# Performance work log

Hardware: AMD Instinct MI355X
Metric: run time of the kernel (lower is better)

Reference implementation:

```python
import jax, jax.numpy as jnp
import numpy as np

EOS = 0
INCLUDE_EOS = True
INS_COST = 1.0
DEL_COST = 1.0
SUB_COST = 1.0


def _seq_lens(tok):
    # tok: (T, N) int tokens; length = index of first EOS (+1 if included), else T
    T = tok.shape[0]
    is_eos = tok == EOS
    has = is_eos.any(axis=0)
    idx = jnp.argmax(is_eos, axis=0)
    return jnp.where(has, idx + (1 if INCLUDE_EOS else 0), T)


def _edit_distance(ref, hyp, ref_lens, hyp_lens):
    # ref: (R, N), hyp: (H, N). Levenshtein DP, scan over hyp steps.
    # The sequential deletion dependence along the ref axis is turned into a
    # min-plus prefix scan: new_row[j] = j*del + cummin_k<=j (cand[k] - k*del).
    R, N = ref.shape
    H = hyp.shape[0]
    offs = (jnp.arange(R + 1, dtype=jnp.float32) * DEL_COST)[:, None]  # (R+1,1)
    row0 = jnp.broadcast_to(offs, (R + 1, N)) + jnp.zeros((R + 1, N), jnp.float32)

    def step(row, xs):
        i, h = xs  # i: 1-based hyp step, h: (N,) hyp tokens at this step
        sub_c = SUB_COST * (ref != h[None, :]).astype(jnp.float32)  # (R,N)
        cand = jnp.concatenate(
            [row[:1] + INS_COST,
             jnp.minimum(row[1:] + INS_COST, row[:-1] + sub_c)], axis=0)
        new_row = jax.lax.cummin(cand - offs, axis=0) + offs
        # freeze rows for sequences whose hypothesis already ended
        row = jnp.where(i <= hyp_lens[None, :], new_row, row)
        return row, None

    row, _ = jax.lax.scan(step, row0, (jnp.arange(1, H + 1), hyp))
    # distance at (hyp_len, ref_len) per sequence
    return jnp.take_along_axis(row, ref_lens[None, :], axis=0)[0]


def setup_inputs() -> dict:
    key = jax.random.key(0)
    k1, k2, k3 = jax.random.split(key, 3)
    log_probs = jax.random.normal(k1, (128, 64), dtype=jnp.float32)
    ref = jax.random.randint(k2, (256, 128), 0, 1000, dtype=jnp.int64)
    hyp = jax.random.randint(k3, (256, 128, 64), 0, 1000, dtype=jnp.int64)
    return {"log_probs": log_probs, "ref": ref, "hyp": hyp}


def reference(log_probs, ref, hyp):
    batch_size, samples = log_probs.shape
    R = ref.shape[0]
    H = hyp.shape[0]
    # ref is 2D: broadcast across samples (same reference per batch element)
    ref_flat = jnp.repeat(ref[:, :, None], samples, axis=2).reshape(R, batch_size * samples)
    hyp_flat = hyp.reshape(H, batch_size * samples)
    ref_lens = _seq_lens(ref_flat)
    hyp_lens = _seq_lens(hyp_flat)
    dist = _edit_distance(ref_flat, hyp_flat, ref_lens, hyp_lens)
    er = dist / ref_lens.astype(jnp.float32)  # norm=True -> error rate
    er = er.reshape(batch_size, samples)
    er = er - er.mean(axis=1, keepdims=True)  # sub_avg=True
    loss = er * jax.nn.softmax(log_probs, axis=1)
    return loss.mean()  # reduction='mean'
```

## Files before the change

kernel.cpp:

```cpp
#include <hip/hip_runtime.h>
#include <stdint.h>


#define BATCH   128
#define SAMPLES 64
#define RLEN    256
#define HLEN    256
#define NSEQ    (BATCH*SAMPLES)
#define NTOK    1000
#define PADTOK  1000
#define SPB     32
#define PMSTR   9
#define HEADPAD 28
#define TAILPAD 40
#define HTROW   324
#define RSTEP   4
#define NPH     72

typedef unsigned long long u64;
typedef unsigned int       u32;

__device__ __forceinline__ int row_shr1(int x) {
    return __builtin_amdgcn_mov_dpp(x, 0x111, 0xf, 0xf, true);
}

__global__ __launch_bounds__(256) void mer_edit(const int* __restrict__ ref,
                                                const int* __restrict__ hyp,
                                                int* __restrict__ scores,
                                                int* __restrict__ reflen)
{
    const int blk  = blockIdx.x;
    const int b    = blk >> 1;
    const int half = blk & 1;
    const int tid  = threadIdx.x;
    const int w    = tid & 7;
    const int sl   = tid >> 3;

    __shared__ __align__(16) u32 pm[9012];
    __shared__ __align__(8)  unsigned short ht[SPB * HTROW];
    __shared__ int m_sh;

    if (tid == 0) m_sh = RLEN;

    for (int i = tid; i < 2253; i += 256)
        ((int4*)pm)[i] = int4{0, 0, 0, 0};

    {
        const int r = tid >> 3, c = tid & 7;
        u32* rowp = (u32*)ht + r * (HTROW / 2);
#pragma unroll
        for (int j0 = 0; j0 < 5; ++j0) {
            int j = c * 5 + j0;
            if (j < 34) {
                int off = (j < 14) ? j : (142 + (j - 14));
                rowp[off] = 0x03E803E8u;
            }
        }
    }

#pragma unroll
    for (int it = 0; it < 8; it++) {
        int idx = it * 256 + tid;
        int t   = idx >> 3;
        int s4  = (idx & 7) * 4;
        int4 v  = *(const int4*)(hyp + t * NSEQ + b * SAMPLES + half * SPB + s4);
        ht[(s4 + 0) * HTROW + HEADPAD + t] = (unsigned short)v.x;
        ht[(s4 + 1) * HTROW + HEADPAD + t] = (unsigned short)v.y;
        ht[(s4 + 2) * HTROW + HEADPAD + t] = (unsigned short)v.z;
        ht[(s4 + 3) * HTROW + HEADPAD + t] = (unsigned short)v.w;
    }

    const int rt = ref[tid * BATCH + b];
    __syncthreads();
    if (rt == 0) atomicMin(&m_sh, tid);
    __syncthreads();
    const int m = (m_sh < RLEN) ? (m_sh + 1) : RLEN;
    if (tid < m)
        atomicOr(&pm[rt * PMSTR + (tid >> 5)], 1u << (tid & 31));
    __syncthreads();

    const int  sw   = (m - 1) >> 5, sb = (m - 1) & 31;
    const bool isW0 = (w == 0);
    const bool isSW = (w == sw);
    const u32* pmw  = pm + w;
    const unsigned short* htrow = ht + sl * HTROW + HEADPAD;

    u32  VP = ~0u, VN = 0u;
    int  score = m;
    bool done  = false;
    int  base  = -(w << 2);

    uint2 tkA = *(const uint2*)(htrow + base);
    uint2 tkB = *(const uint2*)(htrow + base + 4);
    u32 eqA0, eqA1, eqA2, eqA3;
    {
        u32 p0 = tkA.x & 0xFFFFu, p1 = tkA.x >> 16;
        u32 p2 = tkA.y & 0xFFFFu, p3 = tkA.y >> 16;
        eqA0 = pmw[p0 * PMSTR]; eqA1 = pmw[p1 * PMSTR];
        eqA2 = pmw[p2 * PMSTR]; eqA3 = pmw[p3 * PMSTR];
    }

    int out_pkd = 0;

#define STEP(EQ, TK, I) do {                                              \
        u32 cin  = ((u32)inp >> (I)) & 1u;                                \
        u32 hpin = ((u32)inp >> (8 + (I))) & 1u;                          \
        u32 hnin = ((u32)inp >> (16 + (I))) & 1u;                         \
        u32 x  = (EQ) & VP;                                               \
        u64 S  = (u64)x + VP + cin;                                       \
        u32 s2 = (u32)S;                                                  \
        u32 D0 = (s2 ^ VP) | (EQ) | VN;                                   \
        u32 HP = VN | ~(D0 | VP);                                         \
        u32 HN = VP & D0;                                                 \
        nout |= ((u32)(S >> 32) << (I)) | ((HP >> 31) << (8 + (I)))       \
                | ((HN >> 31) << (16 + (I)));                             \
        int delta = (int)((HP >> sb) & 1u) - (int)((HN >> sb) & 1u);      \
        u32 HPs = (HP << 1) | hpin;                                       \
        u32 HNs = (HN << 1) | hnin;                                       \
        VP = HNs | ~(D0 | HPs);                                           \
        VN = HPs & D0;                                                    \
        if (pvalid && !done) score += delta;                              \
        done = done | ((TK) == 0);          \
    } while (0)

#pragma unroll 2
    for (int P = 0; P < NPH; ++P) {
        uint2 tkC = *(const uint2*)(htrow + base + 8);

        u32 n0 = tkB.x & 0xFFFFu, n1 = tkB.x >> 16;
        u32 n2 = tkB.y & 0xFFFFu, n3 = tkB.y >> 16;
        u32 eqB0 = pmw[n0 * PMSTR], eqB1 = pmw[n1 * PMSTR];
        u32 eqB2 = pmw[n2 * PMSTR], eqB3 = pmw[n3 * PMSTR];

        int inp = row_shr1(out_pkd);
        if (isW0) inp = 0x0F00;

        const bool pvalid = ((u32)base < (u32)HLEN);
        u32 nout = 0;
        u32 a0 = tkA.x & 0xFFFFu, a1 = tkA.x >> 16;
        u32 a2 = tkA.y & 0xFFFFu, a3 = tkA.y >> 16;
        STEP(eqA0, a0, 0);
        STEP(eqA1, a1, 1);
        STEP(eqA2, a2, 2);
        STEP(eqA3, a3, 3);
        out_pkd = (int)nout;

        tkA = tkB; tkB = tkC;
        eqA0 = eqB0; eqA1 = eqB1; eqA2 = eqB2; eqA3 = eqB3;
        base += RSTEP;
    }
#undef STEP

    if (isSW) scores[b * SAMPLES + half * SPB + sl] = score;
    if (half == 0 && tid == 0) reflen[b] = m;
}

__global__ __launch_bounds__(64) void mer_loss(const float* __restrict__ lp,
                                               const int* __restrict__ scores,
                                               const int* __restrict__ reflen,
                                               double* __restrict__ partial)
{
    const int b = blockIdx.x, s = threadIdx.x;
    double er = (double)scores[b * SAMPLES + s] / (double)reflen[b];
    double x  = (double)lp[b * SAMPLES + s];
    double mx = x;
#pragma unroll
    for (int off = 32; off > 0; off >>= 1)
        mx = fmax(mx, __shfl_xor(mx, off));
    double e = exp(x - mx);
    double se = e, see = er * e, ser = er;
#pragma unroll
    for (int off = 32; off > 0; off >>= 1) {
        se  += __shfl_xor(se,  off);
        see += __shfl_xor(see, off);
        ser += __shfl_xor(ser, off);
    }
    if (s == 0) partial[b] = see / se - ser * (1.0 / SAMPLES);
}

__global__ __launch_bounds__(64) void mer_final(const double* __restrict__ partial,
                                                float* __restrict__ out)
{
    const int tid = threadIdx.x;
    double v = partial[tid] + partial[tid + 64];
#pragma unroll
    for (int off = 32; off > 0; off >>= 1)
        v += __shfl_xor(v, off);
    if (tid == 0) out[0] = (float)(v / (double)(BATCH * SAMPLES));
}

extern "C" void kernel_launch(void* const* d_in, const int* in_sizes, int n_in,
                              void* d_out, int out_size, void* d_ws, size_t ws_size,
                              hipStream_t stream)
{
    const float* lp  = (const float*)d_in[0];
    const int*   ref = (const int*)d_in[1];
    const int*   hyp = (const int*)d_in[2];

    double* partial = (double*)d_ws;
    int*    scores  = (int*)(partial + BATCH);
    int*    reflen  = scores + NSEQ;
    float*  out     = (float*)d_out;

    mer_edit<<<2 * BATCH, 256, 0, stream>>>(ref, hyp, scores, reflen);
    mer_loss<<<BATCH, 64, 0, stream>>>(lp, scores, reflen, partial);
    mer_final<<<1, 64, 0, stream>>>(partial, out);
}
```

Baseline: 90.02 us.

## Pack hyp LDS stores, precompute hyp length, fuse loss kernels into one

Staging of hypothesis tokens into shared memory now packs two 16-bit tokens per 32-bit store. Each sequence's hypothesis length is computed once before the DP loop, replacing per-step EOS tracking with a bound check. The two small reduction kernels are merged into a single 1024-thread block, removing one launch and the intermediate buffer. The single-block tail serializes the loss over 16 waves.

```diff
diff --git a/kernel.cpp b/kernel.cpp
--- a/kernel.cpp
+++ b/kernel.cpp
@@ -12,7 +12,6 @@
 #define SPB     32
 #define PMSTR   9
 #define HEADPAD 28
-#define TAILPAD 40
 #define HTROW   324
 #define RSTEP   4
 #define NPH     72
@@ -59,15 +58,18 @@
     }
 
 #pragma unroll
-    for (int it = 0; it < 8; it++) {
+    for (int it = 0; it < 4; it++) {
         int idx = it * 256 + tid;
-        int t   = idx >> 3;
+        int p   = idx >> 3;
         int s4  = (idx & 7) * 4;
-        int4 v  = *(const int4*)(hyp + t * NSEQ + b * SAMPLES + half * SPB + s4);
-        ht[(s4 + 0) * HTROW + HEADPAD + t] = (unsigned short)v.x;
-        ht[(s4 + 1) * HTROW + HEADPAD + t] = (unsigned short)v.y;
-        ht[(s4 + 2) * HTROW + HEADPAD + t] = (unsigned short)v.z;
-        ht[(s4 + 3) * HTROW + HEADPAD + t] = (unsigned short)v.w;
+        const int* gp = hyp + b * SAMPLES + half * SPB + s4;
+        int4 v0 = *(const int4*)(gp + (2 * p)     * NSEQ);
+        int4 v1 = *(const int4*)(gp + (2 * p + 1) * NSEQ);
+        u32* col = (u32*)ht + (HEADPAD + 2 * p) / 2;
+        col[(s4 + 0) * (HTROW / 2)] = (u32)(unsigned short)v0.x | ((u32)(unsigned short)v1.x << 16);
+        col[(s4 + 1) * (HTROW / 2)] = (u32)(unsigned short)v0.y | ((u32)(unsigned short)v1.y << 16);
+        col[(s4 + 2) * (HTROW / 2)] = (u32)(unsigned short)v0.z | ((u32)(unsigned short)v1.z << 16);
+        col[(s4 + 3) * (HTROW / 2)] = (u32)(unsigned short)v0.w | ((u32)(unsigned short)v1.w << 16);
     }
 
     const int rt = ref[tid * BATCH + b];
@@ -78,6 +80,23 @@
     if (tid < m)
         atomicOr(&pm[rt * PMSTR + (tid >> 5)], 1u << (tid & 31));
     __syncthreads();
+
+    u32 hlen;
+    {
+        const u32* rowp32 = (const u32*)(ht + sl * HTROW + HEADPAD);
+        int e = 256;
+#pragma unroll
+        for (int j = 0; j < 16; j++) {
+            u32 v  = rowp32[w * 16 + j];
+            int t0 = w * 32 + 2 * j;
+            if ((v & 0xFFFFu) == 0) e = min(e, t0);
+            if ((v >> 16)     == 0) e = min(e, t0 + 1);
+        }
+        e = min(e, __shfl_xor(e, 1));
+        e = min(e, __shfl_xor(e, 2));
+        e = min(e, __shfl_xor(e, 4));
+        hlen = (e < 256) ? (u32)(e + 1) : 256u;
+    }
 
     const int  sw   = (m - 1) >> 5, sb = (m - 1) & 31;
     const bool isW0 = (w == 0);
@@ -87,13 +106,12 @@
 
     u32  VP = ~0u, VN = 0u;
     int  score = m;
-    bool done  = false;
     int  base  = -(w << 2);
 
-    uint2 tkA = *(const uint2*)(htrow + base);
     uint2 tkB = *(const uint2*)(htrow + base + 4);
     u32 eqA0, eqA1, eqA2, eqA3;
     {
+        uint2 tkA = *(const uint2*)(htrow + base);
         u32 p0 = tkA.x & 0xFFFFu, p1 = tkA.x >> 16;
         u32 p2 = tkA.y & 0xFFFFu, p3 = tkA.y >> 16;
         eqA0 = pmw[p0 * PMSTR]; eqA1 = pmw[p1 * PMSTR];
@@ -102,7 +120,7 @@
 
     int out_pkd = 0;
 
-#define STEP(EQ, TK, I) do {                                              \
+#define STEP(EQ, I) do {                                                  \
         u32 cin  = ((u32)inp >> (I)) & 1u;                                \
         u32 hpin = ((u32)inp >> (8 + (I))) & 1u;                          \
         u32 hnin = ((u32)inp >> (16 + (I))) & 1u;                         \
@@ -119,8 +137,7 @@
         u32 HNs = (HN << 1) | hnin;                                       \
         VP = HNs | ~(D0 | HPs);                                           \
         VN = HPs & D0;                                                    \
-        if (pvalid && !done) score += delta;                              \
-        done = done | ((TK) == 0);          \
+        score += ((u32)(base + (I)) < hlen) ? delta : 0;                  \
     } while (0)
 
 #pragma unroll 2
@@ -135,17 +152,14 @@
         int inp = row_shr1(out_pkd);
         if (isW0) inp = 0x0F00;
 
-        const bool pvalid = ((u32)base < (u32)HLEN);
         u32 nout = 0;
-        u32 a0 = tkA.x & 0xFFFFu, a1 = tkA.x >> 16;
-        u32 a2 = tkA.y & 0xFFFFu, a3 = tkA.y >> 16;
-        STEP(eqA0, a0, 0);
-        STEP(eqA1, a1, 1);
-        STEP(eqA2, a2, 2);
-        STEP(eqA3, a3, 3);
+        STEP(eqA0, 0);
+        STEP(eqA1, 1);
+        STEP(eqA2, 2);
+        STEP(eqA3, 3);
         out_pkd = (int)nout;
 
-        tkA = tkB; tkB = tkC;
+        tkB = tkC;
         eqA0 = eqB0; eqA1 = eqB1; eqA2 = eqB2; eqA3 = eqB3;
         base += RSTEP;
     }
@@ -155,38 +169,44 @@
     if (half == 0 && tid == 0) reflen[b] = m;
 }
 
-__global__ __launch_bounds__(64) void mer_loss(const float* __restrict__ lp,
-                                               const int* __restrict__ scores,
-                                               const int* __restrict__ reflen,
-                                               double* __restrict__ partial)
-{
-    const int b = blockIdx.x, s = threadIdx.x;
-    double er = (double)scores[b * SAMPLES + s] / (double)reflen[b];
-    double x  = (double)lp[b * SAMPLES + s];
-    double mx = x;
-#pragma unroll
-    for (int off = 32; off > 0; off >>= 1)
-        mx = fmax(mx, __shfl_xor(mx, off));
-    double e = exp(x - mx);
-    double se = e, see = er * e, ser = er;
-#pragma unroll
-    for (int off = 32; off > 0; off >>= 1) {
-        se  += __shfl_xor(se,  off);
-        see += __shfl_xor(see, off);
-        ser += __shfl_xor(ser, off);
-    }
-    if (s == 0) partial[b] = see / se - ser * (1.0 / SAMPLES);
-}
-
-__global__ __launch_bounds__(64) void mer_final(const double* __restrict__ partial,
-                                                float* __restrict__ out)
+__global__ __launch_bounds__(1024) void mer_tail(const float* __restrict__ lp,
+                                                 const int* __restrict__ scores,
+                                                 const int* __restrict__ reflen,
+                                                 float* __restrict__ out)
 {
     const int tid = threadIdx.x;
-    double v = partial[tid] + partial[tid + 64];
-#pragma unroll
-    for (int off = 32; off > 0; off >>= 1)
-        v += __shfl_xor(v, off);
-    if (tid == 0) out[0] = (float)(v / (double)(BATCH * SAMPLES));
+    const int s   = tid & 63;
+    const int wv  = tid >> 6;
+    __shared__ double red[16];
+
+    double acc = 0.0;
+#pragma unroll
+    for (int k = 0; k < 8; k++) {
+        const int b  = wv * 8 + k;
+        double er = (double)scores[b * SAMPLES + s] / (double)reflen[b];
+        double x  = (double)lp[b * SAMPLES + s];
+        double mx = x;
+#pragma unroll
+        for (int off = 32; off > 0; off >>= 1)
+            mx = fmax(mx, __shfl_xor(mx, off));
+        double e = exp(x - mx);
+        double se = e, see = er * e, ser = er;
+#pragma unroll
+        for (int off = 32; off > 0; off >>= 1) {
+            se  += __shfl_xor(se,  off);
+            see += __shfl_xor(see, off);
+            ser += __shfl_xor(ser, off);
+        }
+        if (s == 0) acc += see / se - ser * (1.0 / SAMPLES);
+    }
+    if (s == 0) red[wv] = acc;
+    __syncthreads();
+    if (tid == 0) {
+        double v = 0.0;
+#pragma unroll
+        for (int i = 0; i < 16; i++) v += red[i];
+        out[0] = (float)(v / (double)(BATCH * SAMPLES));
+    }
 }
 
 extern "C" void kernel_launch(void* const* d_in, const int* in_sizes, int n_in,
@@ -197,12 +217,10 @@
     const int*   ref = (const int*)d_in[1];
     const int*   hyp = (const int*)d_in[2];
 
-    double* partial = (double*)d_ws;
-    int*    scores  = (int*)(partial + BATCH);
-    int*    reflen  = scores + NSEQ;
-    float*  out     = (float*)d_out;
+    int*   scores = (int*)d_ws;
+    int*   reflen = scores + NSEQ;
+    float* out    = (float*)d_out;
 
     mer_edit<<<2 * BATCH, 256, 0, stream>>>(ref, hyp, scores, reflen);
-    mer_loss<<<BATCH, 64, 0, stream>>>(lp, scores, reflen, partial);
-    mer_final<<<1, 64, 0, stream>>>(partial, out);
-}
+    mer_tail<<<1, 1024, 0, stream>>>(lp, scores, reflen, out);
+}
```

After: 103.9 us. 15.4% more time.
